# Performance work log

Hardware: AMD Instinct MI355X
Metric: run time of the kernel (lower is better)

Reference implementation:

```python
import jax, jax.numpy as jnp
import numpy as np

H = 256      # GRU hidden size
E = 768      # embedding_len
H2 = 2 * H   # bidirectional feature dim
NL, NR = 2, 2
DE = (NL + NR) * H2
B, LF = 16, 32


def setup_inputs() -> dict:
    key = jax.random.key(0)
    it = iter(jax.random.split(key, 32))
    def rn(shape, s=0.05):
        return jax.random.normal(next(it), shape, jnp.float32) * s
    return {
        "left_f0": rn((B, LF, E), 1.0),
        "left_f1": rn((B, LF, E), 1.0),
        "right_f0": rn((B, LF, E), 1.0),
        "right_f1": rn((B, LF, E), 1.0),
        "gru_Wih0": rn((2, 3 * H, E)),
        "gru_Whh0": rn((2, 3 * H, H)),
        "gru_bih0": jnp.zeros((2, 3 * H), jnp.float32),
        "gru_bhh0": jnp.zeros((2, 3 * H), jnp.float32),
        "gru_Wih12": rn((2, 2, 3 * H, H2)),
        "gru_Whh12": rn((2, 2, 3 * H, H)),
        "gru_bih12": jnp.zeros((2, 2, 3 * H), jnp.float32),
        "gru_bhh12": jnp.zeros((2, 2, 3 * H), jnp.float32),
        "hwt_Wn": rn((H2, H2)), "hwt_bn": jnp.zeros((H2,), jnp.float32),
        "hwt_Wg": rn((H2, H2)), "hwt_bg": jnp.full((H2,), -2.0, jnp.float32),
        "lint_W": rn((1, H2)), "lint_b": jnp.zeros((1,), jnp.float32),
        "attr_left": rn((NL, H2)), "attr_right": rn((NR, H2)),
        "empty_attr": rn((H2,)),
        "hwe_Wn": rn((DE, DE)), "hwe_bn": jnp.zeros((DE,), jnp.float32),
        "hwe_Wg": rn((DE, DE)), "hwe_bg": jnp.full((DE,), -2.0, jnp.float32),
        "line_W": rn((2, DE)),
        "line_b": jnp.full((2,), float(-np.log(0.99 / 0.01)), jnp.float32),
    }


def _gru_layer(x, Wih, Whh, bih, bhh, reverse):
    # x: [B,T,D] -> [B,T,H], PyTorch GRU gate order (r, z, n)
    xi = jnp.einsum('btd,gd->btg', x, Wih) + bih
    xi = jnp.swapaxes(xi, 0, 1)  # [T,B,3H]
    h0 = jnp.zeros((x.shape[0], H), x.dtype)
    def step(h, xt):
        gh = h @ Whh.T + bhh
        ir, iz, inn = jnp.split(xt, 3, axis=-1)
        hr, hz, hn = jnp.split(gh, 3, axis=-1)
        r = jax.nn.sigmoid(ir + hr)
        z = jax.nn.sigmoid(iz + hz)
        n = jnp.tanh(inn + r * hn)
        h_new = (1 - z) * n + z * h
        return h_new, h_new
    _, ys = jax.lax.scan(step, h0, xi, reverse=reverse)
    return jnp.swapaxes(ys, 0, 1)


def _masked_softmax(x, mask, axis):
    return jax.nn.softmax(x + jnp.where(mask, 0.0, -1e10), axis=axis)


def _highway(x, Wn, bn, Wg, bg):
    n = jax.nn.relu(x @ Wn.T + bn)
    g = jax.nn.sigmoid(x @ Wg.T + bg)
    return n * g + (1 - g) * x


def reference(left_f0, left_f1, right_f0, right_f1,
              gru_Wih0, gru_Whh0, gru_bih0, gru_bhh0,
              gru_Wih12, gru_Whh12, gru_bih12, gru_bhh12,
              hwt_Wn, hwt_bn, hwt_Wg, hwt_bg, lint_W, lint_b,
              attr_left, attr_right, empty_attr,
              hwe_Wn, hwe_bn, hwe_Wg, hwe_bg, line_W, line_b):
    def bigru(x):
        f = _gru_layer(x, gru_Wih0[0], gru_Whh0[0], gru_bih0[0], gru_bhh0[0], False)
        b = _gru_layer(x, gru_Wih0[1], gru_Whh0[1], gru_bih0[1], gru_bhh0[1], True)
        h = jnp.concatenate([f, b], -1)
        for l in range(2):
            f = _gru_layer(h, gru_Wih12[l, 0], gru_Whh12[l, 0], gru_bih12[l, 0], gru_bhh12[l, 0], False)
            b = _gru_layer(h, gru_Wih12[l, 1], gru_Whh12[l, 1], gru_bih12[l, 1], gru_bhh12[l, 1], True)
            h = jnp.concatenate([f, b], -1)
        return h  # [B,T,2H]

    left_fields = [left_f0, left_f1]
    right_fields = [right_f0, right_f1]
    left_emb = [bigru(v) for v in left_fields]
    right_emb = [bigru(v) for v in right_fields]

    def masks(fields):
        tm = [jnp.sum(v != 0, axis=2) > 0 for v in fields]
        am = [jnp.sum(m, axis=1, keepdims=True) > 0 for m in tm]
        return jnp.concatenate(tm, 1), jnp.concatenate(am, 1)

    l_tok_mask, l_attr_mask = masks(left_fields)
    r_tok_mask, r_attr_mask = masks(right_fields)

    def token_matching(Le, Re, r_mask):
        L = jnp.concatenate(Le, 1)
        R = jnp.concatenate(Re, 1)
        cm = jnp.abs(L[:, :, None, :] - R[:, None, :, :])   # [B,L,R,2H]
        hw = _highway(cm, hwt_Wn, hwt_bn, hwt_Wg, hwt_bg)
        scores = hw @ lint_W.T + lint_b                     # [B,L,R,1]
        w = _masked_softmax(scores, r_mask[:, None, :, None], axis=2)
        return jnp.sum(cm * w, axis=2)                      # [B,L,2H]

    l_cmp = token_matching(left_emb, right_emb, r_tok_mask)
    r_cmp = token_matching(right_emb, left_emb, l_tok_mask)

    def attribute_matching(embs, attr_emb, cmp_res, tok_mask, attr_mask):
        start, res = 0, []
        for i, v in enumerate(embs):
            Lf = v.shape[1]
            m = tok_mask[:, start:start + Lf]               # [B,Lf]
            w = _masked_softmax(v @ attr_emb[i], m, axis=1)[:, :, None]
            res.append(jnp.sum(cmp_res[:, start:start + Lf] * w, axis=1))
            start += Lf
        res = jnp.stack(res, axis=1)                        # [B,nf,2H]
        return jnp.where(attr_mask[:, :, None], res, empty_attr)

    l_rep = attribute_matching(left_emb, attr_left, l_cmp, l_tok_mask, l_attr_mask)
    r_rep = attribute_matching(right_emb, attr_right, r_cmp, r_tok_mask, r_attr_mask)

    concat = jnp.concatenate([l_rep, r_rep], axis=1).reshape(l_rep.shape[0], -1)
    hw = _highway(concat, hwe_Wn, hwe_bn, hwe_Wg, hwe_bg)
    out = hw @ line_W.T + line_b
    return jax.nn.log_softmax(out, axis=1)
```

## Files before the change

### kernel.cpp

```cpp
#include <hip/hip_runtime.h>
#include <hip/hip_bf16.h>

#define NH 256
#define NE 768
#define NH2 512
#define NG3 768
#define NB 16
#define NLF 32
#define NBT 2048
#define NDE 2048

typedef short s16x8 __attribute__((ext_vector_type(8)));
typedef float f32x4 __attribute__((ext_vector_type(4)));

#define TK_SWZ(g, r) (((g) + ((r) >> 1)) & 3)

#if __has_builtin(__builtin_amdgcn_global_load_lds)
#define GLOAD_LDS16(gp, lp) \
  __builtin_amdgcn_global_load_lds((const __attribute__((address_space(1))) unsigned int*)(gp), \
                                   (__attribute__((address_space(3))) unsigned int*)(lp), 16, 0, 0)
#define HAVE_GLLDS 1
#else
#define HAVE_GLLDS 0
#endif

__device__ __forceinline__ float fsig_(float x){
  return __builtin_amdgcn_rcpf(1.f + __expf(-x));
}
__device__ __forceinline__ float ftanh_(float x){
  float e = __expf(2.f*x);
  return 1.f - 2.f*__builtin_amdgcn_rcpf(e + 1.f);
}
__device__ __forceinline__ unsigned short f2bf_(float f){
  unsigned int x = __float_as_uint(f);
  unsigned int r = (x + 0x7fffu + ((x>>16)&1u)) >> 16;
  return (unsigned short)r;
}
__device__ __forceinline__ float bfx_(unsigned int u){ return __uint_as_float(u << 16); }
__device__ __forceinline__ unsigned int pack_bf16_rnd(float a, float b){
  unsigned int ua = __float_as_uint(a) + 0x8000u;
  unsigned int ub = __float_as_uint(b) + 0x8000u;
  return __builtin_amdgcn_perm(ub, ua, 0x07060302u);
}
__device__ __forceinline__ int tokrow(int side, int b, int tok){
  return (((side*2 + (tok>>5))*16 + b) << 5) + (tok & 31);
}

__global__ void k_gather(const float* __restrict__ f0, const float* __restrict__ f1,
                         const float* __restrict__ f2, const float* __restrict__ f3,
                         float* __restrict__ X0){
  int m = blockIdx.x;
  int f = m >> 9, rem = m & 511;
  const float* src = (f==0)? f0 : (f==1)? f1 : (f==2)? f2 : f3;
  const float* sp = src + (size_t)rem*NE;
  float* dp = X0 + (size_t)m*NE;
  for (int d = threadIdx.x; d < NE; d += 256) dp[d] = sp[d];
}

__global__ void k_masks(const float* __restrict__ f0, const float* __restrict__ f1,
                        const float* __restrict__ f2, const float* __restrict__ f3,
                        float* __restrict__ TM, float* __restrict__ AM){
  int f = blockIdx.x, b = blockIdx.y;
  const float* src = (f==0)? f0 : (f==1)? f1 : (f==2)? f2 : f3;
  __shared__ unsigned int flags[33];
  if (threadIdx.x < 33) flags[threadIdx.x] = 0u;
  __syncthreads();
  for (int t = 0; t < 32; t++){
    const float* row = src + ((size_t)b*NLF + t)*NE;
    bool nz = false;
    for (int d = threadIdx.x; d < NE; d += 256) nz |= (row[d] != 0.f);
    if (nz) atomicOr(&flags[t], 1u);
  }
  __syncthreads();
  int side = f >> 1, fi = f & 1;
  if (threadIdx.x < 32){
    unsigned int fl = flags[threadIdx.x];
    TM[side*1024 + b*64 + fi*32 + threadIdx.x] = fl ? 1.f : 0.f;
    if (fl) atomicOr(&flags[32], 1u);
  }
  __syncthreads();
  if (threadIdx.x == 0) AM[side*32 + b*2 + fi] = flags[32] ? 1.f : 0.f;
}

__global__ void k_prep_whh(const float* __restrict__ w0, const float* __restrict__ w12,
                           unsigned short* __restrict__ dst){
  int idx = blockIdx.x*256 + threadIdx.x;
  float v = (idx < 393216) ? w0[idx] : w12[idx - 393216];
  dst[idx] = f2bf_(v);
}

__global__ void k_prep_tw(const float* __restrict__ Wn, const float* __restrict__ Wg,
                          unsigned short* __restrict__ TW){
  int idx = blockIdx.x*256 + threadIdx.x;
  int kpos = idx & 31;
  int n    = (idx >> 5) & 127;
  int kc   = (idx >> 12) & 15;
  int nc   = idx >> 16;
  int gpos = kpos >> 3, j = kpos & 7;
  int gorig = (gpos - (n>>1)) & 3;
  int k = kc*32 + gorig*8 + j;
  int q = n >> 1, type = n & 1;
  const float* src = type ? Wg : Wn;
  TW[idx] = f2bf_(src[(size_t)(nc*64 + q)*NH2 + k]);
}

template<bool ABF16>
__global__ __launch_bounds__(256) void k_gemm_mfma(
    const void* __restrict__ Av,
    const float* __restrict__ Wb, long wsz,
    const float* __restrict__ biasb, long bsz,
    unsigned short* __restrict__ XIo, long csz,
    int K)
{
  int z = blockIdx.z;
  const float* W = Wb + (size_t)z*wsz;
  const float* bias = biasb + (size_t)z*bsz;
  unsigned short* XO = XIo + (size_t)z*csz;
  int n0 = blockIdx.x*128, m0 = blockIdx.y*128;
  __shared__ short At[128*32];
  __shared__ short Wt[128*32];
  int tid = threadIdx.x;
  int wave = tid >> 6, wm = wave >> 1, wn = wave & 1;
  int lane = tid & 63, l15 = lane & 15, lq = lane >> 4;
  int sm = tid & 127, gb = (tid >> 7) * 2;

  f32x4 zero4 = {0.f,0.f,0.f,0.f};
  f32x4 acc[4][4];
  #pragma unroll
  for (int mi=0;mi<4;mi++)
    #pragma unroll
    for (int nj=0;nj<4;nj++) acc[mi][nj] = zero4;

  const float* wr = W + (size_t)(n0 + sm)*K;

  for (int k0 = 0; k0 < K; k0 += 32){
    if constexpr (ABF16){
      const unsigned short* ar = (const unsigned short*)Av + (size_t)(m0 + sm)*K;
      #pragma unroll
      for (int gi = 0; gi < 2; gi++){
        int g = gb + gi;
        *(uint4*)&At[sm*32 + TK_SWZ(g,sm)*8] = *(const uint4*)&ar[k0 + g*8];
      }
    } else {
      const float* ar = (const float*)Av + (size_t)(m0 + sm)*K;
      #pragma unroll
      for (int gi = 0; gi < 2; gi++){
        int g = gb + gi;
        const float* ap = ar + k0 + g*8;
        float4 a0 = *(const float4*)ap, a1 = *(const float4*)(ap+4);
        uint4 pa = { pack_bf16_rnd(a0.x,a0.y), pack_bf16_rnd(a0.z,a0.w),
                     pack_bf16_rnd(a1.x,a1.y), pack_bf16_rnd(a1.z,a1.w) };
        *(uint4*)&At[sm*32 + TK_SWZ(g,sm)*8] = pa;
      }
    }
    #pragma unroll
    for (int gi = 0; gi < 2; gi++){
      int g = gb + gi;
      const float* wp = wr + k0 + g*8;
      float4 w0 = *(const float4*)wp, w1 = *(const float4*)(wp+4);
      uint4 pw = { pack_bf16_rnd(w0.x,w0.y), pack_bf16_rnd(w0.z,w0.w),
                   pack_bf16_rnd(w1.x,w1.y), pack_bf16_rnd(w1.z,w1.w) };
      *(uint4*)&Wt[sm*32 + TK_SWZ(g,sm)*8] = pw;
    }
    __syncthreads();
    s16x8 af[4], wf[4];
    #pragma unroll
    for (int mi=0;mi<4;mi++){
      int row = wm*64 + mi*16 + l15;
      af[mi] = *(const s16x8*)&At[row*32 + TK_SWZ(lq,row)*8];
    }
    #pragma unroll
    for (int nj=0;nj<4;nj++){
      int row = wn*64 + nj*16 + l15;
      wf[nj] = *(const s16x8*)&Wt[row*32 + TK_SWZ(lq,row)*8];
    }
    #pragma unroll
    for (int mi=0;mi<4;mi++)
      #pragma unroll
      for (int nj=0;nj<4;nj++)
        acc[mi][nj] = __builtin_amdgcn_mfma_f32_16x16x32_bf16(af[mi], wf[nj], acc[mi][nj], 0,0,0);
    __syncthreads();
  }
  #pragma unroll
  for (int nj=0;nj<4;nj++){
    int n = n0 + wn*64 + nj*16 + l15;
    float bv = bias[n];
    #pragma unroll
    for (int mi=0;mi<4;mi++){
      int mbase = m0 + wm*64 + mi*16 + lq*4;
      #pragma unroll
      for (int r=0;r<4;r++){
        int m = mbase + r;
        int t = m & 31, bp = m >> 5;
        XO[((size_t)(t*64 + bp))*NG3 + n] = f2bf_(acc[mi][nj][r] + bv);
      }
    }
  }
}

__device__ __forceinline__ void loadxi_(const unsigned short* __restrict__ rowp,
                                        int lq, unsigned int* arr){
  #pragma unroll
  for (int p = 0; p < 2; p++)
    #pragma unroll
    for (int gg = 0; gg < 3; gg++)
      #pragma unroll
      for (int r4 = 0; r4 < 4; r4++)
        arr[(p*3+gg)*4 + r4] = rowp[(lq*4 + r4)*NG3 + gg*256 + p*128];
}

__global__ __launch_bounds__(512, 2) void k_scan_mfma(
    const unsigned short* __restrict__ xi,
    const unsigned short* __restrict__ whh,
    const float* __restrict__ bhhb, long bhh_stride,
    unsigned short* __restrict__ Hout,
    int chain0)
{
  int g = blockIdx.x;
  int dir = blockIdx.y;
  int tid = threadIdx.x;
  int w = tid >> 6;
  int lane = tid & 63, l15 = lane & 15, lq = lane >> 4;
  const unsigned short* W = whh + (size_t)(chain0 + dir)*NG3*NH;
  const float* bhh = bhhb + (size_t)dir*bhh_stride;
  const unsigned short* xid = xi + (size_t)dir*(32*64*NG3);
  int b0 = g*16;

  __shared__ unsigned short hbuf[2*16*264];
  for (int i = tid; i < 2*16*264; i += 512) hbuf[i] = 0;

  unsigned int xc[24], xn[24];
  {
    int t0 = dir ? 31 : 0;
    loadxi_(xid + (size_t)(t0*64 + b0)*NG3 + 16*w + l15, lq, xc);
  }

  s16x8 warr[6][8];
  #pragma unroll
  for (int p6 = 0; p6 < 6; p6++){
    const unsigned short* wp = W + (size_t)(16*(w + 8*p6) + l15)*NH + lq*8;
    #pragma unroll
    for (int kt = 0; kt < 8; kt++)
      warr[p6][kt] = *(const s16x8*)(wp + kt*32);
  }
  float brv[2], bzv[2], bnv[2];
  #pragma unroll
  for (int p = 0; p < 2; p++){
    int u = p*128 + 16*w + l15;
    brv[p] = bhh[u]; bzv[p] = bhh[256+u]; bnv[p] = bhh[512+u];
  }
  float hreg[2][4] = {{0,0,0,0},{0,0,0,0}};
  __syncthreads();

  for (int s = 0; s < 32; s++){
    int t = dir ? (31 - s) : s;
    int cur = s & 1, nxt = cur ^ 1;
    const unsigned short* rbp = hbuf + cur*4224;
    unsigned short* wbp = hbuf + nxt*4224;

    if (s < 31){
      int tn = dir ? (31 - (s+1)) : (s+1);
      loadxi_(xid + (size_t)(tn*64 + b0)*NG3 + 16*w + l15, lq, xn);
    }

    f32x4 acc[6];
    #pragma unroll
    for (int p6 = 0; p6 < 6; p6++) acc[p6] = (f32x4){0.f,0.f,0.f,0.f};
    #pragma unroll
    for (int kt = 0; kt < 8; kt++){
      s16x8 a = *(const s16x8*)&rbp[l15*264 + kt*32 + lq*8];
      #pragma unroll
      for (int p6 = 0; p6 < 6; p6++)
        acc[p6] = __builtin_amdgcn_mfma_f32_16x16x32_bf16(a, warr[p6][kt], acc[p6], 0,0,0);
    }

    #pragma unroll
    for (int p = 0; p < 2; p++){
      int u = p*128 + 16*w + l15;
      #pragma unroll
      for (int r4 = 0; r4 < 4; r4++){
        int m = lq*4 + r4;
        float xr_ = bfx_(xc[(p*3+0)*4 + r4]);
        float xz_ = bfx_(xc[(p*3+1)*4 + r4]);
        float xn_ = bfx_(xc[(p*3+2)*4 + r4]);
        float rr = fsig_(xr_ + acc[p][r4]   + brv[p]);
        float zz = fsig_(xz_ + acc[2+p][r4] + bzv[p]);
        float nn = ftanh_(xn_ + rr*(acc[4+p][r4] + bnv[p]));
        float hnew = (1.f - zz)*nn + zz*hreg[p][r4];
        hreg[p][r4] = hnew;
        unsigned short hb = f2bf_(hnew);
        wbp[m*264 + u] = hb;
        Hout[((size_t)(b0 + m)*32 + t)*NH2 + dir*256 + u] = hb;
      }
    }
    #pragma unroll
    for (int i = 0; i < 24; i++) xc[i] = xn[i];
    __syncthreads();
  }
}

__global__ __launch_bounds__(256) void k_cm_pretile(
    const unsigned short* __restrict__ Hf, unsigned short* __restrict__ CMT, int b0)
{
  int ip = blockIdx.x, bl = blockIdx.y;
  int b = b0 + bl;
  int tid = threadIdx.x;
  int m = tid & 127, gb = (tid >> 7) * 2;
  int i_ = ip*2 + (m >> 6), j_ = m & 63;
  const unsigned short* Lrow = Hf + (size_t)tokrow(0, b, i_)*NH2;
  const unsigned short* Rrow = Hf + (size_t)tokrow(1, b, j_)*NH2;
  unsigned short* dst = CMT + ((size_t)(bl*32 + ip) * 16) * 4096;
  for (int kc = 0; kc < 16; kc++){
    int k0 = kc*32;
    #pragma unroll
    for (int gi = 0; gi < 2; gi++){
      int g = gb + gi;
      uint4 lu = *(const uint4*)&Lrow[k0 + g*8];
      uint4 ru = *(const uint4*)&Rrow[k0 + g*8];
      unsigned int lw[4] = {lu.x, lu.y, lu.z, lu.w};
      unsigned int rw[4] = {ru.x, ru.y, ru.z, ru.w};
      uint4 pk;
      unsigned int pr[4];
      #pragma unroll
      for (int q = 0; q < 4; q++){
        float la = __uint_as_float(lw[q] << 16), lb = __uint_as_float(lw[q] & 0xffff0000u);
        float ra = __uint_as_float(rw[q] << 16), rb = __uint_as_float(rw[q] & 0xffff0000u);
        pr[q] = pack_bf16_rnd(fabsf(la - ra), fabsf(lb - rb));
      }
      pk.x = pr[0]; pk.y = pr[1]; pk.z = pr[2]; pk.w = pr[3];
      *(uint4*)&dst[kc*4096 + m*32 + TK_SWZ(g,m)*8] = pk;
    }
  }
}

__global__ __launch_bounds__(256) void k_token_mfma(
    const unsigned short* __restrict__ CMT,
    const unsigned short* __restrict__ TW,
    const float* __restrict__ bn, const float* __restrict__ bg,
    const float* __restrict__ lintW,
    float* __restrict__ P, int b0)
{
  __shared__ short Atile[4096];
  __shared__ short Btile[4096];
  __shared__ short Asave[8192];
  __shared__ float sred[256];
  int ip = blockIdx.x, bl = blockIdx.y, nc = blockIdx.z;
  int b = b0 + bl;
  int tid = threadIdx.x;
  int wave = tid >> 6, wm = wave >> 1, wn = wave & 1;
  int lane = tid & 63, l15 = lane & 15, lq = lane >> 4;

  const char* Ab = (const char*)(CMT + ((size_t)(bl*32 + ip) * 16) * 4096);
  const char* Bb = (const char*)(TW + ((size_t)(nc*16)) * 4096);

  f32x4 zero4 = {0.f,0.f,0.f,0.f};
  f32x4 acc[4][4];
  #pragma unroll
  for (int mi=0;mi<4;mi++)
    #pragma unroll
    for (int nj=0;nj<4;nj++) acc[mi][nj] = zero4;

  for (int kc = 0; kc < 16; kc++){
    const char* gA = Ab + (size_t)kc*8192;
    const char* gB = Bb + (size_t)kc*8192;
#if HAVE_GLLDS
    char* lA = (char*)Atile + wave*1024;
    char* lB = (char*)Btile + wave*1024;
    GLOAD_LDS16(gA + tid*16, lA);
    GLOAD_LDS16(gA + 4096 + tid*16, lA + 4096);
    GLOAD_LDS16(gB + tid*16, lB);
    GLOAD_LDS16(gB + 4096 + tid*16, lB + 4096);
    int cs = kc - 2*nc;
    if ((unsigned)cs < 2u){
      char* lS = (char*)Asave + cs*8192 + wave*1024;
      GLOAD_LDS16(gA + tid*16, lS);
      GLOAD_LDS16(gA + 4096 + tid*16, lS + 4096);
    }
#else
    {
      uint4 va0 = ((const uint4*)gA)[tid], va1 = ((const uint4*)gA)[256+tid];
      uint4 vb0 = ((const uint4*)gB)[tid], vb1 = ((const uint4*)gB)[256+tid];
      ((uint4*)Atile)[tid] = va0; ((uint4*)Atile)[256+tid] = va1;
      ((uint4*)Btile)[tid] = vb0; ((uint4*)Btile)[256+tid] = vb1;
      int cs = kc - 2*nc;
      if ((unsigned)cs < 2u){
        ((uint4*)Asave)[cs*512 + tid] = va0; ((uint4*)Asave)[cs*512 + 256+tid] = va1;
      }
    }
#endif
    __syncthreads();
    s16x8 af[4], bfv[4];
    #pragma unroll
    for (int mi=0;mi<4;mi++){
      int row = wm*64 + mi*16 + l15;
      af[mi] = *(const s16x8*)&Atile[row*32 + TK_SWZ(lq,row)*8];
    }
    #pragma unroll
    for (int nj=0;nj<4;nj++){
      int row = wn*64 + nj*16 + l15;
      bfv[nj] = *(const s16x8*)&Btile[row*32 + TK_SWZ(lq,row)*8];
    }
    #pragma unroll
    for (int mi=0;mi<4;mi++)
      #pragma unroll
      for (int nj=0;nj<4;nj++)
        acc[mi][nj] = __builtin_amdgcn_mfma_f32_16x16x32_bf16(af[mi], bfv[nj], acc[mi][nj], 0,0,0);
    __syncthreads();
  }

  float bnv[4], bgv[4], lwv[4]; int qv[4];
  #pragma unroll
  for (int nj=0;nj<4;nj++){
    int q = (wn*64 + nj*16 + l15) >> 1;
    qv[nj] = q;
    int nf = nc*64 + q;
    bnv[nj] = bn[nf]; bgv[nj] = bg[nf]; lwv[nj] = lintW[nf];
  }
  float lmask = (l15 & 1) ? 0.f : 1.f;
  float sc[4][4];
  #pragma unroll
  for (int mi=0;mi<4;mi++)
    #pragma unroll
    for (int r=0;r<4;r++) sc[mi][r] = 0.f;

  #pragma unroll
  for (int nj=0;nj<4;nj++){
    int q = qv[nj];
    int cs = q >> 5, kk = q & 31, gor = kk >> 3, el = kk & 7;
    #pragma unroll
    for (int mi=0;mi<4;mi++){
      int mbase = wm*64 + mi*16 + lq*4;
      #pragma unroll
      for (int r=0;r<4;r++){
        float v  = acc[mi][nj][r];
        float pv = __shfl_xor(v, 1);
        int mm = mbase + r;
        unsigned short cu = (unsigned short)Asave[cs*4096 + mm*32 + TK_SWZ(gor,mm)*8 + el];
        float cmf = __uint_as_float(((unsigned int)cu) << 16);
        float an = v + bnv[nj];
        float gg = fsig_(pv + bgv[nj]);
        float hw = fmaxf(an, 0.f)*gg + (1.f - gg)*cmf;
        sc[mi][r] += lmask * lwv[nj] * hw;
      }
    }
  }
  #pragma unroll
  for (int mi=0;mi<4;mi++)
    #pragma unroll
    for (int r=0;r<4;r++){
      float v = sc[mi][r];
      v += __shfl_xor(v, 1); v += __shfl_xor(v, 2);
      v += __shfl_xor(v, 4); v += __shfl_xor(v, 8);
      sc[mi][r] = v;
    }
  if (l15 == 0){
    #pragma unroll
    for (int mi=0;mi<4;mi++)
      #pragma unroll
      for (int r=0;r<4;r++)
        sred[(wm*64 + mi*16 + lq*4 + r)*2 + wn] = sc[mi][r];
  }
  __syncthreads();
  if (tid < 128){
    float v = sred[tid*2] + sred[tid*2+1];
    int isel = tid >> 6, j = tid & 63;
    P[(((size_t)nc*16 + b)*64 + (ip*2 + isel))*64 + j] = v;
  }
}

__global__ void k_score_reduce(const float* __restrict__ P, float* __restrict__ S){
  int idx = blockIdx.x*256 + threadIdx.x;
  float v = 0.f;
  #pragma unroll
  for (int nc = 0; nc < 8; nc++) v += P[(size_t)nc*65536 + idx];
  S[idx] = v;
}

__global__ void k_softmax_wl(const float* __restrict__ S, const float* __restrict__ TM,
                             float* __restrict__ WLo){
  int i = blockIdx.x, b = blockIdx.y, j = threadIdx.x;
  float mask = TM[1024 + b*64 + j];
  float v = S[((size_t)b*64 + i)*64 + j] + (mask != 0.f ? 0.f : -1e10f);
  float m = v;
  for (int o = 32; o; o >>= 1) m = fmaxf(m, __shfl_xor(m, o));
  float e = __expf(v - m), s = e;
  for (int o = 32; o; o >>= 1) s += __shfl_xor(s, o);
  WLo[((size_t)b*64 + i)*64 + j] = e / s;
}
__global__ void k_softmax_wr(const float* __restrict__ S, const float* __restrict__ TM,
                             float* __restrict__ WRo){
  int j = blockIdx.x, b = blockIdx.y, i = threadIdx.x;
  float mask = TM[b*64 + i];
  float v = S[((size_t)b*64 + i)*64 + j] + (mask != 0.f ? 0.f : -1e10f);
  float m = v;
  for (int o = 32; o; o >>= 1) m = fmaxf(m, __shfl_xor(m, o));
  float e = __expf(v - m), s = e;
  for (int o = 32; o; o >>= 1) s += __shfl_xor(s, o);
  WRo[((size_t)b*64 + j)*64 + i] = e / s;
}

__global__ __launch_bounds__(256) void k_cmp(const unsigned short* __restrict__ Hf,
    const float* __restrict__ w, float* __restrict__ out, int side){
  int p = blockIdx.x, b = blockIdx.y;
  __shared__ float wl[64];
  if (threadIdx.x < 64) wl[threadIdx.x] = w[((size_t)b*64 + p)*64 + threadIdx.x];
  __syncthreads();
  int xr = tokrow(side, b, p);
  int d1 = threadIdx.x, d2 = threadIdx.x + 256;
  float x1 = bfx_(Hf[(size_t)xr*NH2 + d1]), x2 = bfx_(Hf[(size_t)xr*NH2 + d2]);
  float a1 = 0.f, a2 = 0.f;
  for (int q = 0; q < 64; q++){
    const unsigned short* yr = Hf + (size_t)tokrow(side^1, b, q)*NH2;
    float wq = wl[q];
    a1 += wq * fabsf(x1 - bfx_(yr[d1]));
    a2 += wq * fabsf(x2 - bfx_(yr[d2]));
  }
  out[((size_t)b*64 + p)*NH2 + d1] = a1;
  out[((size_t)b*64 + p)*NH2 + d2] = a2;
}

__global__ __launch_bounds__(256) void k_attr(const unsigned short* __restrict__ Hf,
    const float* __restrict__ attrL, const float* __restrict__ attrR,
    const float* __restrict__ LC, const float* __restrict__ RC,
    const float* __restrict__ TM, const float* __restrict__ AM,
    const float* __restrict__ emptyA, float* __restrict__ CC){
  int fi = blockIdx.x, b = blockIdx.y, side = blockIdx.z;
  const float* attr = (side ? attrR : attrL) + fi*512;
  const float* cmp = side ? RC : LC;
  __shared__ float sc[32], wv[32];
  int t = threadIdx.x >> 3, l8 = threadIdx.x & 7;
  const unsigned short* er = Hf + (size_t)tokrow(side, b, fi*32 + t)*NH2;
  float acc = 0.f;
  for (int d = l8*64; d < l8*64 + 64; d++) acc += bfx_(er[d])*attr[d];
  acc += __shfl_down(acc, 4, 8);
  acc += __shfl_down(acc, 2, 8);
  acc += __shfl_down(acc, 1, 8);
  if (l8 == 0) sc[t] = acc;
  __syncthreads();
  if (threadIdx.x < 32){
    float mask = TM[side*1024 + b*64 + fi*32 + threadIdx.x];
    float v = sc[threadIdx.x] + (mask != 0.f ? 0.f : -1e10f);
    float m = v;
    for (int o = 16; o; o >>= 1) m = fmaxf(m, __shfl_xor(m, o, 32));
    float e = __expf(v - m), s = e;
    for (int o = 16; o; o >>= 1) s += __shfl_xor(s, o, 32);
    wv[threadIdx.x] = e / s;
  }
  __syncthreads();
  float am = AM[side*32 + b*2 + fi];
  int d1 = threadIdx.x, d2 = threadIdx.x + 256;
  float a1 = 0.f, a2 = 0.f;
  for (int t2 = 0; t2 < 32; t2++){
    float wq = wv[t2];
    const float* cr = cmp + ((size_t)b*64 + fi*32 + t2)*NH2;
    a1 += wq * cr[d1];
    a2 += wq * cr[d2];
  }
  float* dst = CC + (size_t)b*NDE + (size_t)(side*2 + fi)*512;
  dst[d1] = (am != 0.f) ? a1 : emptyA[d1];
  dst[d2] = (am != 0.f) ? a2 : emptyA[d2];
}

__global__ __launch_bounds__(256) void k_final_hw(const float* __restrict__ X,
    const float* __restrict__ Wn, const float* __restrict__ bn,
    const float* __restrict__ Wg, const float* __restrict__ bg,
    float* __restrict__ HWo){
  __shared__ float Xs[4][2048];
  int nb = blockIdx.x, bq = blockIdx.y;
  for (int idx = threadIdx.x; idx < 8192; idx += 256)
    Xs[idx>>11][idx & 2047] = X[(size_t)(bq*4 + (idx>>11))*NDE + (idx & 2047)];
  __syncthreads();
  int nl = threadIdx.x >> 1, kl = threadIdx.x & 1;
  int n = nb*128 + nl;
  const float* wnr = Wn + (size_t)n*NDE + kl*1024;
  const float* wgr = Wg + (size_t)n*NDE + kl*1024;
  float an[4] = {0,0,0,0}, ag[4] = {0,0,0,0};
  for (int k = 0; k < 1024; k++){
    float wn = wnr[k], wg = wgr[k];
    int kk = kl*1024 + k;
    #pragma unroll
    for (int b4 = 0; b4 < 4; b4++){
      float xv = Xs[b4][kk];
      an[b4] = fmaf(wn, xv, an[b4]);
      ag[b4] = fmaf(wg, xv, ag[b4]);
    }
  }
  #pragma unroll
  for (int b4 = 0; b4 < 4; b4++){
    an[b4] += __shfl_down(an[b4], 1);
    ag[b4] += __shfl_down(ag[b4], 1);
  }
  if (kl == 0){
    float bnv = bn[n], bgv = bg[n];
    #pragma unroll
    for (int b4 = 0; b4 < 4; b4++){
      float a = an[b4] + bnv;
      float g = fsig_(ag[b4] + bgv);
      float xv = Xs[b4][n];
      HWo[(size_t)(bq*4 + b4)*NDE + n] = fmaxf(a, 0.f)*g + (1.f - g)*xv;
    }
  }
}

__global__ void k_out(const float* __restrict__ HWi, const float* __restrict__ lw,
                      const float* __restrict__ lb, float* __restrict__ out){
  int b = blockIdx.x, lane = threadIdx.x;
  float p0 = 0.f, p1 = 0.f;
  for (int n = lane; n < 2048; n += 64){
    float h = HWi[(size_t)b*NDE + n];
    p0 += h * lw[n];
    p1 += h * lw[2048 + n];
  }
  for (int o = 32; o; o >>= 1){ p0 += __shfl_xor(p0, o); p1 += __shfl_xor(p1, o); }
  if (lane == 0){
    float o0 = p0 + lb[0], o1 = p1 + lb[1];
    float m = fmaxf(o0, o1);
    float lse = m + logf(expf(o0 - m) + expf(o1 - m));
    out[b*2]   = o0 - lse;
    out[b*2+1] = o1 - lse;
  }
}

extern "C" void kernel_launch(void* const* d_in, const int* in_sizes, int n_in,
                              void* d_out, int out_size, void* d_ws, size_t ws_size,
                              hipStream_t stream){
  const float* lf0 = (const float*)d_in[0];
  const float* lf1 = (const float*)d_in[1];
  const float* rf0 = (const float*)d_in[2];
  const float* rf1 = (const float*)d_in[3];
  const float* gWih0 = (const float*)d_in[4];
  const float* gWhh0 = (const float*)d_in[5];
  const float* gbih0 = (const float*)d_in[6];
  const float* gbhh0 = (const float*)d_in[7];
  const float* gWih12 = (const float*)d_in[8];
  const float* gWhh12 = (const float*)d_in[9];
  const float* gbih12 = (const float*)d_in[10];
  const float* gbhh12 = (const float*)d_in[11];
  const float* hwtWn = (const float*)d_in[12];
  const float* hwtbn = (const float*)d_in[13];
  const float* hwtWg = (const float*)d_in[14];
  const float* hwtbg = (const float*)d_in[15];
  const float* lintW = (const float*)d_in[16];
  const float* attrL = (const float*)d_in[18];
  const float* attrR = (const float*)d_in[19];
  const float* emptyA = (const float*)d_in[20];
  const float* hweWn = (const float*)d_in[21];
  const float* hwebn = (const float*)d_in[22];
  const float* hweWg = (const float*)d_in[23];
  const float* hwebg = (const float*)d_in[24];
  const float* lineW = (const float*)d_in[25];
  const float* lineB = (const float*)d_in[26];
  float* out = (float*)d_out;

  unsigned short* HA = (unsigned short*)d_ws;
  unsigned short* HB = HA + 1048576;
  unsigned short* WHH = HB + 1048576;
  unsigned short* TW  = WHH + 1179648;
  float* Sb  = (float*)(TW + 524288);
  float* WLb = Sb  + 65536;
  float* WRb = WLb + 65536;
  float* LC  = WRb + 65536;
  float* RC  = LC + 524288;
  float* TM  = RC + 524288;
  float* AM  = TM + 2048;
  float* CC  = AM + 64;
  float* HWb = CC + 32768;
  float* P   = HWb + 32768;
  unsigned short* CMT = (unsigned short*)(P + 524288);
  float* X0 = (float*)CMT;
  unsigned short* XI = (unsigned short*)(X0 + 1572864);

  k_gather<<<NBT, 256, 0, stream>>>(lf0, lf1, rf0, rf1, X0);
  k_masks<<<dim3(4,16), 256, 0, stream>>>(lf0, lf1, rf0, rf1, TM, AM);
  k_prep_whh<<<4608, 256, 0, stream>>>(gWhh0, gWhh12, WHH);
  k_prep_tw<<<2048, 256, 0, stream>>>(hwtWn, hwtWg, TW);

  const long XSZ = 1572864;
  k_gemm_mfma<false><<<dim3(6,16,2), 256, 0, stream>>>(X0, gWih0, (long)NG3*NE, gbih0, NG3,
                                                       XI, XSZ, NE);
  k_scan_mfma<<<dim3(4,2), 512, 0, stream>>>(XI, WHH, gbhh0, NG3, HA, 0);
  k_gemm_mfma<true><<<dim3(6,16,2), 256, 0, stream>>>(HA, gWih12, (long)NG3*NH2, gbih12, NG3,
                                                      XI, XSZ, NH2);
  k_scan_mfma<<<dim3(4,2), 512, 0, stream>>>(XI, WHH, gbhh12, NG3, HB, 2);
  k_gemm_mfma<true><<<dim3(6,16,2), 256, 0, stream>>>(HB, gWih12 + (size_t)2*NG3*NH2, (long)NG3*NH2,
                                                      gbih12 + 2*NG3, NG3,
                                                      XI, XSZ, NH2);
  k_scan_mfma<<<dim3(4,2), 512, 0, stream>>>(XI, WHH, gbhh12 + 2*NG3, NG3, HA, 4);

  for (int c = 0; c < 4; c++){
    k_cm_pretile<<<dim3(32,4), 256, 0, stream>>>(HA, CMT, c*4);
    k_token_mfma<<<dim3(32,4,8), 256, 0, stream>>>(CMT, TW, hwtbn, hwtbg, lintW, P, c*4);
  }
  k_score_reduce<<<256, 256, 0, stream>>>(P, Sb);
  k_softmax_wl<<<dim3(64,16), 64, 0, stream>>>(Sb, TM, WLb);
  k_softmax_wr<<<dim3(64,16), 64, 0, stream>>>(Sb, TM, WRb);
  k_cmp<<<dim3(64,16), 256, 0, stream>>>(HA, WLb, LC, 0);
  k_cmp<<<dim3(64,16), 256, 0, stream>>>(HA, WRb, RC, 1);

  k_attr<<<dim3(2,16,2), 256, 0, stream>>>(HA, attrL, attrR, LC, RC, TM, AM, emptyA, CC);

  k_final_hw<<<dim3(16,4), 256, 0, stream>>>(CC, hweWn, hwebn, hweWg, hwebg, HWb);
  k_out<<<16, 64, 0, stream>>>(HWb, lineW, lineB, out);
}
```

Measured before the change: 842.4 us.

## Store GRU input projections in per-thread scan order for vectorized loads

The input-projection GEMM epilogue now writes its bf16 results in a layout permuted to match each scan thread's exact consumption order, 24 contiguous values per thread per timestep. The recurrent scan kernel then fetches them with three 16-byte vector loads instead of 24 scattered 2-byte loads each step. This targets the latency and transaction count of the per-step input loads on the sequential critical path. The GEMM's stores become more scattered, and the two kernels are now tightly coupled through the index mapping.

```diff
diff --git a/kernel.cpp b/kernel.cpp
--- a/kernel.cpp
+++ b/kernel.cpp
@@ -44,6 +44,11 @@
 }
 __device__ __forceinline__ int tokrow(int side, int b, int tok){
   return (((side*2 + (tok>>5))*16 + b) << 5) + (tok & 31);
+}
+__device__ __forceinline__ float xiget_(const uint4* x4, int idx){
+  const unsigned int* w = (const unsigned int*)x4;
+  unsigned int v = w[idx >> 1];
+  return (idx & 1) ? __uint_as_float(v & 0xffff0000u) : __uint_as_float(v << 16);
 }
 
 __global__ void k_gather(const float* __restrict__ f0, const float* __restrict__ f1,
@@ -185,28 +190,23 @@
   for (int nj=0;nj<4;nj++){
     int n = n0 + wn*64 + nj*16 + l15;
     float bv = bias[n];
+    int gg = n >> 8;
+    int u256 = n & 255;
+    int p = u256 >> 7, w_s = (u256 >> 4) & 7, l15_s = u256 & 15;
+    int cofs = (p*3 + gg)*4;
     #pragma unroll
     for (int mi=0;mi<4;mi++){
       int mbase = m0 + wm*64 + mi*16 + lq*4;
-      #pragma unroll
-      for (int r=0;r<4;r++){
-        int m = mbase + r;
-        int t = m & 31, bp = m >> 5;
-        XO[((size_t)(t*64 + bp))*NG3 + n] = f2bf_(acc[mi][nj][r] + bv);
-      }
-    }
-  }
-}
-
-__device__ __forceinline__ void loadxi_(const unsigned short* __restrict__ rowp,
-                                        int lq, unsigned int* arr){
-  #pragma unroll
-  for (int p = 0; p < 2; p++)
-    #pragma unroll
-    for (int gg = 0; gg < 3; gg++)
-      #pragma unroll
-      for (int r4 = 0; r4 < 4; r4++)
-        arr[(p*3+gg)*4 + r4] = rowp[(lq*4 + r4)*NG3 + gg*256 + p*128];
+      int t0 = mbase & 31, bp = mbase >> 5;
+      int g = bp >> 4, mloc = bp & 15;
+      int lq_s = mloc >> 2, r4 = mloc & 3;
+      int tid_s = w_s*64 + lq_s*16 + l15_s;
+      size_t base = ((size_t)(t0*4 + g)*512 + tid_s)*24 + cofs + r4;
+      #pragma unroll
+      for (int r=0;r<4;r++)
+        XO[base + (size_t)r*49152] = f2bf_(acc[mi][nj][r] + bv);
+    }
+  }
 }
 
 __global__ __launch_bounds__(512, 2) void k_scan_mfma(
@@ -223,16 +223,17 @@
   int lane = tid & 63, l15 = lane & 15, lq = lane >> 4;
   const unsigned short* W = whh + (size_t)(chain0 + dir)*NG3*NH;
   const float* bhh = bhhb + (size_t)dir*bhh_stride;
-  const unsigned short* xid = xi + (size_t)dir*(32*64*NG3);
+  const unsigned short* xid = xi + (size_t)dir*1572864;
   int b0 = g*16;
 
   __shared__ unsigned short hbuf[2*16*264];
   for (int i = tid; i < 2*16*264; i += 512) hbuf[i] = 0;
 
-  unsigned int xc[24], xn[24];
+  uint4 xc4[3], xn4[3];
   {
     int t0 = dir ? 31 : 0;
-    loadxi_(xid + (size_t)(t0*64 + b0)*NG3 + 16*w + l15, lq, xc);
+    const uint4* p0 = (const uint4*)(xid + ((size_t)(t0*4 + g)*512 + tid)*24);
+    xc4[0] = p0[0]; xc4[1] = p0[1]; xc4[2] = p0[2];
   }
 
   s16x8 warr[6][8];
@@ -260,7 +261,8 @@
 
     if (s < 31){
       int tn = dir ? (31 - (s+1)) : (s+1);
-      loadxi_(xid + (size_t)(tn*64 + b0)*NG3 + 16*w + l15, lq, xn);
+      const uint4* pn = (const uint4*)(xid + ((size_t)(tn*4 + g)*512 + tid)*24);
+      xn4[0] = pn[0]; xn4[1] = pn[1]; xn4[2] = pn[2];
     }
 
     f32x4 acc[6];
@@ -280,9 +282,9 @@
       #pragma unroll
       for (int r4 = 0; r4 < 4; r4++){
         int m = lq*4 + r4;
-        float xr_ = bfx_(xc[(p*3+0)*4 + r4]);
-        float xz_ = bfx_(xc[(p*3+1)*4 + r4]);
-        float xn_ = bfx_(xc[(p*3+2)*4 + r4]);
+        float xr_ = xiget_(xc4, (p*3+0)*4 + r4);
+        float xz_ = xiget_(xc4, (p*3+1)*4 + r4);
+        float xn_ = xiget_(xc4, (p*3+2)*4 + r4);
         float rr = fsig_(xr_ + acc[p][r4]   + brv[p]);
         float zz = fsig_(xz_ + acc[2+p][r4] + bzv[p]);
         float nn = ftanh_(xn_ + rr*(acc[4+p][r4] + bnv[p]));
@@ -293,8 +295,9 @@
         Hout[((size_t)(b0 + m)*32 + t)*NH2 + dir*256 + u] = hb;
       }
     }
-    #pragma unroll
-    for (int i = 0; i < 24; i++) xc[i] = xn[i];
+    if (s < 31){
+      xc4[0] = xn4[0]; xc4[1] = xn4[1]; xc4[2] = xn4[2];
+    }
     __syncthreads();
   }
 }
```

Result: faster. 809.9 us (-3.9%).
